# Performance work log

Measured on AMD Instinct MI355X. Metric: run time of the kernel, lower is better.

The kernel has to match this reference:

```python
import jax, jax.numpy as jnp
import numpy as np

H = 8
HID = 512
DH = HID // H
EPS = 1e-5


def _ln(x, g, b):
    mu = jnp.mean(x, axis=-1, keepdims=True)
    var = jnp.mean(jnp.square(x - mu), axis=-1, keepdims=True)
    return (x - mu) * jax.lax.rsqrt(var + EPS) * g + b


def setup_inputs() -> dict:
    key = jax.random.key(0)
    ks = jax.random.split(key, 40)
    L, M, P, D = 4096, 1024, 4096, 512

    def xav(k, shp):
        lim = np.sqrt(6.0 / (shp[0] + shp[1]))
        return jax.random.uniform(k, shp, jnp.float32, -lim, lim)

    inp = {
        'lncRNA_embedding': jax.random.normal(ks[0], (L, D), jnp.float32),
        'miRNA_embedding': jax.random.normal(ks[1], (M, D), jnp.float32),
        'protein_embedding': jax.random.normal(ks[2], (P, D), jnp.float32),
        'lncRNA_miRNA_matrix': jax.random.randint(ks[3], (L, M), 0, 2, jnp.int32),
        'protein_miRNA_matrix': jax.random.randint(ks[4], (P, M), 0, 2, jnp.int32),
    }
    names = ['Wl', 'Wm', 'Wp', 'Wql', 'Wkl', 'Wvl', 'Wqp', 'Wkp', 'Wvp']
    for i, n in enumerate(names):
        inp[n] = xav(ks[5 + i], (HID, HID))
        inp['b' + n[1:]] = jnp.zeros((HID,), jnp.float32)
    inp['Wml'] = xav(ks[20], (2 * HID, D // 2))
    inp['bml'] = jnp.zeros((D // 2,), jnp.float32)
    inp['Wmp'] = xav(ks[21], (2 * HID, D // 2))
    inp['bmp'] = jnp.zeros((D // 2,), jnp.float32)
    inp['g1'] = jnp.ones((D // 2,), jnp.float32)
    inp['be1'] = jnp.zeros((D // 2,), jnp.float32)
    inp['g2'] = jnp.ones((D // 2,), jnp.float32)
    inp['be2'] = jnp.zeros((D // 2,), jnp.float32)
    # first three linears take dim-D input (D == HID here)
    return inp


def reference(lncRNA_embedding, miRNA_embedding, protein_embedding,
              lncRNA_miRNA_matrix, protein_miRNA_matrix,
              Wl, bl, Wm, bm, Wp, bp,
              Wql, bql, Wkl, bkl, Wvl, bvl,
              Wqp, bqp, Wkp, bkp, Wvp, bvp,
              Wml, bml, Wmp, bmp, g1, be1, g2, be2):
    L = lncRNA_embedding.shape[0]
    M = miRNA_embedding.shape[0]
    P = protein_embedding.shape[0]

    lt = lncRNA_embedding @ Wl + bl          # [L, HID]
    mt = miRNA_embedding @ Wm + bm           # [M, HID]
    pt = protein_embedding @ Wp + bp         # [P, HID]

    def heads(x, W, b, n):
        return (x @ W + b).reshape(n, H, DH)

    Ql = heads(lt, Wql, bql, L)              # [L, H, DH]
    Kl = heads(mt, Wkl, bkl, M)
    Vl = heads(mt, Wvl, bvl, M)
    Qp = heads(pt, Wqp, bqp, P)
    Kp = heads(mt, Wkp, bkp, M)
    Vp = heads(mt, Wvp, bvp, M)

    scale = 1.0 / np.sqrt(DH)
    sl = jnp.einsum('lhd,mhd->hlm', Ql, Kl) * scale      # [H, L, M]
    sl = jnp.where(lncRNA_miRNA_matrix[None] == 0, -1e9, sl)
    awl = jax.nn.softmax(sl, axis=-1)

    sp = jnp.einsum('phd,mhd->hpm', Qp, Kp) * scale      # [H, P, M]
    sp = jnp.where(protein_miRNA_matrix[None] == 0, -1e9, sp)
    awp = jax.nn.softmax(sp, axis=-1)

    ctx_l = jax.nn.relu(jnp.einsum('hlm,mhd->lhd', awl, Vl).reshape(L, HID))
    ctx_p = jax.nn.relu(jnp.einsum('hpm,mhd->phd', awp, Vp).reshape(P, HID))

    mutual = jnp.einsum('hlm,hpm->lp', awl, awp) / H     # [L, P]

    fin_l = ctx_l + mutual @ ctx_p
    fin_p = ctx_p + mutual.T @ ctx_l

    out_l = _ln(jnp.concatenate([lt, fin_l], axis=-1) @ Wml + bml, g1, be1)
    out_p = _ln(jnp.concatenate([fin_p, pt], axis=-1) @ Wmp + bmp, g2, be2)
    return out_l, out_p
```

## Files before the change

kernel.cpp:

```cpp
#include <hip/hip_runtime.h>
#include <hip/hip_bf16.h>

using bf16 = __hip_bfloat16;
typedef __attribute__((ext_vector_type(8))) short short8;
typedef __attribute__((ext_vector_type(4))) float floatx4;
typedef __attribute__((ext_vector_type(8))) unsigned short ushort8;
typedef __attribute__((ext_vector_type(4))) int i32x4;
typedef __attribute__((ext_vector_type(8))) int i32x8;

__device__ __forceinline__ float b2f(unsigned short u) {
    union { unsigned int i; float f; } x; x.i = ((unsigned int)u) << 16; return x.f;
}

__device__ __forceinline__ void async16(const void* g, void* l) {
    __builtin_amdgcn_global_load_lds((const __attribute__((address_space(1))) void*)g,
                                     (__attribute__((address_space(3))) void*)l,
                                     16, 0, 0);
}

__device__ __forceinline__ unsigned char f2e4m3(float f) {
    unsigned s = (__float_as_uint(f) >> 24) & 0x80u;
    f = fminf(fabsf(f), 448.f);
    if (f < 0.015625f) {
        int d = (int)rintf(f * 512.f);
        return (unsigned char)(s | (unsigned)d);
    }
    int E = (int)((__float_as_uint(f) >> 23) & 255u) - 127;
    float ulp_inv = __uint_as_float((unsigned)(127 + 3 - E) << 23);
    int m = (int)rintf(f * ulp_inv);
    int n = (m == 16) ? ((E + 8) << 3) : (((E + 7) << 3) + (m - 8));
    if (n > 0x7E) n = 0x7E;
    return (unsigned char)(s | (unsigned)n);
}

__device__ __forceinline__ unsigned int pk4_e4m3(float a, float b, float c, float d) {
#if __has_builtin(__builtin_amdgcn_cvt_pk_fp8_f32)
    int p = __builtin_amdgcn_cvt_pk_fp8_f32(a, b, 0, false);
    p = __builtin_amdgcn_cvt_pk_fp8_f32(c, d, p, true);
    return (unsigned int)p;
#else
    return (unsigned)f2e4m3(a) | ((unsigned)f2e4m3(b) << 8) |
           ((unsigned)f2e4m3(c) << 16) | ((unsigned)f2e4m3(d) << 24);
#endif
}

__device__ __forceinline__ bool sniff_wave(const unsigned short* p) {
    const int lane = threadIdx.x & 63;
    int wild = 0;
#pragma unroll
    for (int j = 0; j < 4; ++j) {
        float a = fabsf(b2f(p[lane * 4 + j]));
        wild += !(a <= 1e4f);
    }
#pragma unroll
    for (int o = 1; o < 64; o <<= 1) wild += __shfl_xor(wild, o);
    return wild > 16;
}

struct Cvt { const void* src; bf16* dst; int n; };
struct PrepArgs {
    Cvt cv[18];
    const void* tsrc[11];
    bf16* tdst[11];
    const int* msrc[2];
    unsigned char* mdst[2];
    const unsigned short* sn;
};

__global__ __launch_bounds__(256) void prep(PrepArgs a) {
    const int y = blockIdx.y;
    __shared__ bf16 tile[32][33];

    if (y >= 29) {
        const int* src = a.msrc[y - 29];
        unsigned char* dst = a.mdst[y - 29];
        const int n = 4096 * 1024;
        const int stride = gridDim.x * 256 * 16;
        for (int i = (blockIdx.x * 256 + threadIdx.x) * 16; i < n; i += stride) {
            union { unsigned char b[16]; i32x4 v; } u;
#pragma unroll
            for (int j = 0; j < 4; ++j) {
                i32x4 m = *(const i32x4*)(src + i + j * 4);
#pragma unroll
                for (int k = 0; k < 4; ++k) u.b[j * 4 + k] = m[k] ? 1 : 0;
            }
            *(i32x4*)(dst + i) = u.v;
        }
        return;
    }

    const bool f32 = sniff_wave(a.sn);
    if (y < 18) {
        const Cvt c = a.cv[y];
        const int stride = gridDim.x * 256 * 8;
        for (int i = (blockIdx.x * 256 + threadIdx.x) * 8; i < c.n; i += stride) {
            if (f32) {
                const float* s = (const float*)c.src + i;
#pragma unroll
                for (int j = 0; j < 8; ++j) c.dst[i + j] = __float2bfloat16(s[j]);
            } else {
                *(ushort8*)((unsigned short*)c.dst + i) =
                    *(const ushort8*)((const unsigned short*)c.src + i);
            }
        }
        return;
    }

    const int tx = threadIdx.x & 31;
    const int ty = threadIdx.x >> 5;
    if (y < 27) {
        const void* in = a.tsrc[y - 18];
        bf16* out = a.tdst[y - 18];
        const int bc = (blockIdx.x & 15) * 32;
        const int br = (blockIdx.x >> 4) * 32;
#pragma unroll
        for (int i = 0; i < 32; i += 8) {
            const size_t idx = (size_t)(br + ty + i) * 512 + bc + tx;
            tile[ty + i][tx] = f32 ? __float2bfloat16(((const float*)in)[idx])
                                   : ((const bf16*)in)[idx];
        }
        __syncthreads();
#pragma unroll
        for (int i = 0; i < 32; i += 8)
            out[(size_t)(bc + ty + i) * 512 + br + tx] = tile[tx][ty + i];
    } else {
        const void* in = a.tsrc[y - 27 + 9];
        bf16* out = a.tdst[y - 27 + 9];
        const int bc = (blockIdx.x & 7) * 32;
        const int br = (blockIdx.x >> 3) * 32;
#pragma unroll
        for (int i = 0; i < 32; i += 8) {
            const size_t idx = (size_t)(br + ty + i) * 256 + bc + tx;
            tile[ty + i][tx] = f32 ? __float2bfloat16(((const float*)in)[idx])
                                   : ((const bf16*)in)[idx];
        }
        __syncthreads();
#pragma unroll
        for (int i = 0; i < 32; i += 8)
            out[(size_t)(bc + ty + i) * 1024 + br + tx] = tile[tx][ty + i];
    }
}

struct SegTab { const bf16* W[3]; const bf16* bias[3]; bf16* C[3]; int ldc[3]; int rs[3]; };

__global__ __launch_bounds__(256) void gemm_bt_seg(
    const bf16* __restrict__ A, SegTab T, int K)
{
    constexpr int TM = 2, TN = 2;
    __align__(16) __shared__ bf16 As[64 * 64];
    __align__(16) __shared__ bf16 Bs[64 * 64];

    const int lane = threadIdx.x & 63;
    const int wv   = threadIdx.x >> 6;
    const int gm   = blockIdx.y * 64;
    const int seg  = (gm >= 5120) ? 2 : ((gm >= 4096) ? 1 : 0);
    const bf16* B  = T.W[seg];
    const bf16* bias = T.bias[seg];
    bf16* C        = T.C[seg];
    const int ldc  = T.ldc[seg];
    const int m_base = gm - T.rs[seg];
    const int n_base = blockIdx.x * 64;
    const int wm0 = (wv >> 1) * 32;
    const int wn0 = (wv & 1) * 32;

    floatx4 zero = {0.f, 0.f, 0.f, 0.f};
    floatx4 acc[TM][TN];
#pragma unroll
    for (int mt = 0; mt < TM; ++mt)
#pragma unroll
        for (int nt = 0; nt < TN; ++nt) acc[mt][nt] = zero;

    const int sr  = lane >> 3;
    const int sce = ((lane & 7) ^ sr) * 8;
    const int fr  = lane & 15;
    const int q   = lane >> 4;
    const int sw  = fr & 7;

    for (int k0 = 0; k0 < K; k0 += 64) {
#pragma unroll
        for (int cc = 0; cc < 2; ++cc) {
            const int r0t = (wv + cc * 4) * 8;
            async16(A + (size_t)(gm + r0t + sr) * 512 + k0 + sce, &As[r0t * 64]);
            async16(B + (size_t)(n_base + r0t + sr) * 512 + k0 + sce, &Bs[r0t * 64]);
        }
        __syncthreads();
#pragma unroll
        for (int s = 0; s < 2; ++s) {
            const int off = ((s * 4 + q) ^ sw) * 8;
            short8 af[TM], bfr[TN];
#pragma unroll
            for (int mt = 0; mt < TM; ++mt)
                af[mt] = *(const short8*)&As[(wm0 + mt * 16 + fr) * 64 + off];
#pragma unroll
            for (int nt = 0; nt < TN; ++nt)
                bfr[nt] = *(const short8*)&Bs[(wn0 + nt * 16 + fr) * 64 + off];
#pragma unroll
            for (int mt = 0; mt < TM; ++mt)
#pragma unroll
                for (int nt = 0; nt < TN; ++nt)
                    acc[mt][nt] = __builtin_amdgcn_mfma_f32_16x16x32_bf16(
                        af[mt], bfr[nt], acc[mt][nt], 0, 0, 0);
        }
        __syncthreads();
    }

    const int er = lane >> 4;
    const int ec = lane & 15;
#pragma unroll
    for (int nt = 0; nt < TN; ++nt) {
        const int col = n_base + wn0 + nt * 16 + ec;
        const float bv = __bfloat162float(bias[col]);
#pragma unroll
        for (int mt = 0; mt < TM; ++mt)
#pragma unroll
            for (int r = 0; r < 4; ++r) {
                const int row = m_base + wm0 + mt * 16 + er * 4 + r;
                C[(size_t)row * ldc + col] = __float2bfloat16(acc[mt][nt][r] + bv);
            }
    }
}

struct BtArgs { const bf16* A; const bf16* B; void* C; const bf16* bias;
                int lda, ldb, ldc; };
struct BtSet { BtArgs s[3]; };

template <bool F32OUT, bool REMAP2>
__global__ __launch_bounds__(256) void gemm_btx(BtSet P, int K, float scale)
{
    constexpr int TM = 2, TN = 2;
    __align__(16) __shared__ bf16 As[64 * 64];
    __align__(16) __shared__ bf16 Bs[64 * 64];

    const BtArgs g = P.s[blockIdx.z];
    int bx = blockIdx.x, by = blockIdx.y;
    if (REMAP2 && blockIdx.z == 2) {
        const int flat = by * gridDim.x + bx;
        bx = flat & 31; by = flat >> 5;
    }
    const int lane = threadIdx.x & 63;
    const int wv   = threadIdx.x >> 6;
    const int m_base = by * 64;
    const int n_base = bx * 64;
    const int wm0 = (wv >> 1) * 32;
    const int wn0 = (wv & 1) * 32;

    floatx4 zero = {0.f, 0.f, 0.f, 0.f};
    floatx4 acc[TM][TN];
#pragma unroll
    for (int mt = 0; mt < TM; ++mt)
#pragma unroll
        for (int nt = 0; nt < TN; ++nt) acc[mt][nt] = zero;

    const int sr  = lane >> 3;
    const int sce = ((lane & 7) ^ sr) * 8;
    const int fr  = lane & 15;
    const int q   = lane >> 4;
    const int sw  = fr & 7;

    for (int k0 = 0; k0 < K; k0 += 64) {
#pragma unroll
        for (int cc = 0; cc < 2; ++cc) {
            const int r0t = (wv + cc * 4) * 8;
            async16(g.A + (size_t)(m_base + r0t + sr) * g.lda + k0 + sce, &As[r0t * 64]);
            async16(g.B + (size_t)(n_base + r0t + sr) * g.ldb + k0 + sce, &Bs[r0t * 64]);
        }
        __syncthreads();
#pragma unroll
        for (int s = 0; s < 2; ++s) {
            const int off = ((s * 4 + q) ^ sw) * 8;
            short8 af[TM], bfr[TN];
#pragma unroll
            for (int mt = 0; mt < TM; ++mt)
                af[mt] = *(const short8*)&As[(wm0 + mt * 16 + fr) * 64 + off];
#pragma unroll
            for (int nt = 0; nt < TN; ++nt)
                bfr[nt] = *(const short8*)&Bs[(wn0 + nt * 16 + fr) * 64 + off];
#pragma unroll
            for (int mt = 0; mt < TM; ++mt)
#pragma unroll
                for (int nt = 0; nt < TN; ++nt)
                    acc[mt][nt] = __builtin_amdgcn_mfma_f32_16x16x32_bf16(
                        af[mt], bfr[nt], acc[mt][nt], 0, 0, 0);
        }
        __syncthreads();
    }

    const int er = lane >> 4;
    const int ec = lane & 15;
#pragma unroll
    for (int nt = 0; nt < TN; ++nt) {
        const int col = n_base + wn0 + nt * 16 + ec;
        const float bv = __bfloat162float(g.bias[col]);
#pragma unroll
        for (int mt = 0; mt < TM; ++mt)
#pragma unroll
            for (int r = 0; r < 4; ++r) {
                const int row = m_base + wm0 + mt * 16 + er * 4 + r;
                const float v = acc[mt][nt][r] * scale + bv;
                if constexpr (F32OUT)
                    ((float*)g.C)[(size_t)row * g.ldc + col] = v;
                else
                    ((bf16*)g.C)[(size_t)row * g.ldc + col] = __float2bfloat16(v);
            }
    }
}

struct ScArgs { const bf16* Q; const bf16* K; const unsigned char* mask;
                unsigned char* aw; unsigned char* awt; };
struct ScSet { ScArgs s[2]; const bf16* vsrc[2]; unsigned char* vdst[2]; };

__global__ __launch_bounds__(256) void scores_v8(ScSet P, int ldk, float scale)
{
    __shared__ float wred[16][4];
    __shared__ float wsum[16][4];
    __shared__ float tile[32][33];

    const int flat = blockIdx.x;
    if (flat >= 4096) {
        const int f2   = flat - 4096;
        const int side = f2 >> 9;
        const int rem  = f2 & 511;
        const bf16* in = P.vsrc[side];
        unsigned char* out = P.vdst[side];
        const int bc = (rem & 15) * 32;
        const int br = (rem >> 4) * 32;
        const int tx = threadIdx.x & 31;
        const int ty = threadIdx.x >> 5;
#pragma unroll
        for (int i = 0; i < 32; i += 8)
            tile[ty + i][tx] =
                __bfloat162float(in[(size_t)(br + ty + i) * 2048 + bc + tx]) * 4.0f;
        __syncthreads();
        const unsigned int vp = pk4_e4m3(tile[tx][ty], tile[tx][ty + 8],
                                         tile[tx][ty + 16], tile[tx][ty + 24]);
#pragma unroll
        for (int i = 0; i < 4; ++i)
            out[(size_t)(bc + ty + i * 8) * 1024 + br + tx] =
                (unsigned char)(vp >> (8 * i));
        return;
    }

    const int side = flat >> 11;
    const int idx  = flat & 2047;
    const int h    = idx & 7;
    const int r0   = (idx >> 3) * 16;

    const ScArgs g = P.s[side];
    const int t    = threadIdx.x;
    const int lane = t & 63;
    const int w    = t >> 6;
    const int fr   = lane & 15;
    const int fq   = lane >> 4;
    const int cbase = w * 256;

    const short* Qs = (const short*)g.Q + (size_t)(r0 + fr) * 512 + h * 64 + fq * 8;
    short8 a0 = *(const short8*)(Qs);
    short8 a1 = *(const short8*)(Qs + 32);

    floatx4 accs[16];
    const short* Kb = (const short*)g.K + h * 64 + fq * 8;
#pragma unroll
    for (int c = 0; c < 16; ++c) {
        const int krow = cbase + c * 16 + fr;
        short8 b0 = *(const short8*)(Kb + (size_t)krow * ldk);
        short8 b1 = *(const short8*)(Kb + (size_t)krow * ldk + 32);
        floatx4 acc = {0.f, 0.f, 0.f, 0.f};
        acc = __builtin_amdgcn_mfma_f32_16x16x32_bf16(a0, b0, acc, 0, 0, 0);
        acc = __builtin_amdgcn_mfma_f32_16x16x32_bf16(a1, b1, acc, 0, 0, 0);
        accs[c] = acc;
    }

    float mxr[4] = {-3e38f, -3e38f, -3e38f, -3e38f};
#pragma unroll
    for (int c = 0; c < 16; ++c) {
        const int col = cbase + c * 16 + fr;
#pragma unroll
        for (int r = 0; r < 4; ++r) {
            const int row = r0 + fq * 4 + r;
            float v = (g.mask[(size_t)row * 1024 + col] == 0) ? -1e9f
                                                              : accs[c][r] * scale;
            accs[c][r] = v;
            mxr[r] = fmaxf(mxr[r], v);
        }
    }
#pragma unroll
    for (int o = 1; o < 16; o <<= 1)
#pragma unroll
        for (int r = 0; r < 4; ++r) mxr[r] = fmaxf(mxr[r], __shfl_xor(mxr[r], o));
    if (fr == 0)
#pragma unroll
        for (int r = 0; r < 4; ++r) wred[fq * 4 + r][w] = mxr[r];
    __syncthreads();

    float mx[4], sm[4] = {0.f, 0.f, 0.f, 0.f};
#pragma unroll
    for (int r = 0; r < 4; ++r) {
        const int row = fq * 4 + r;
        mx[r] = fmaxf(fmaxf(wred[row][0], wred[row][1]),
                      fmaxf(wred[row][2], wred[row][3]));
    }
#pragma unroll
    for (int c = 0; c < 16; ++c)
#pragma unroll
        for (int r = 0; r < 4; ++r) {
            float e = __expf(accs[c][r] - mx[r]);
            accs[c][r] = e;
            sm[r] += e;
        }
#pragma unroll
    for (int o = 1; o < 16; o <<= 1)
#pragma unroll
        for (int r = 0; r < 4; ++r) sm[r] += __shfl_xor(sm[r], o);
    if (fr == 0)
#pragma unroll
        for (int r = 0; r < 4; ++r) wsum[fq * 4 + r][w] = sm[r];
    __syncthreads();

    float inv[4];
#pragma unroll
    for (int r = 0; r < 4; ++r) {
        const int row = fq * 4 + r;
        inv[r] = 32.0f / (wsum[row][0] + wsum[row][1] + wsum[row][2] + wsum[row][3]);
    }
    unsigned char* awtb = g.awt + (size_t)(r0 >> 4) * 131072 + fq * 4;
#pragma unroll
    for (int c = 0; c < 16; ++c) {
        const int col = cbase + c * 16 + fr;
        const unsigned int pk = pk4_e4m3(accs[c][0] * inv[0], accs[c][1] * inv[1],
                                         accs[c][2] * inv[2], accs[c][3] * inv[3]);
#pragma unroll
        for (int r = 0; r < 4; ++r)
            g.aw[(size_t)(r0 + fq * 4 + r) * 8192 + h * 1024 + col] =
                (unsigned char)(pk >> (8 * r));
        *(unsigned int*)(awtb + (size_t)(h * 1024 + col) * 16) = pk;
    }
}

struct B8Args { const unsigned char* A; const unsigned char* B; bf16* C;
                unsigned char* CT; };
struct B8Pair { B8Args s[2]; };

__global__ __launch_bounds__(256) void gemm_bt8_ctx(
    B8Pair P, int lda, long long a_kshift, int ldb, int ldc, int ldct,
    int K, float scale)
{
    constexpr int TM = 2, TN = 2;
    __align__(16) __shared__ unsigned char As[2][64 * 64];
    __align__(16) __shared__ unsigned char Bs[2][64 * 64];

    const B8Args g = P.s[blockIdx.z];
    const int lane = threadIdx.x & 63;
    const int wv   = threadIdx.x >> 6;
    const int m_base = blockIdx.y * 64;
    const int n_base = blockIdx.x * 64;
    const unsigned char* A = g.A + (long long)blockIdx.x * a_kshift;

    const int wm0 = (wv >> 1) * 32;
    const int wn0 = (wv & 1) * 32;

    floatx4 zero = {0.f, 0.f, 0.f, 0.f};
    floatx4 acc[TM][TN];
#pragma unroll
    for (int mt = 0; mt < TM; ++mt)
#pragma unroll
        for (int nt = 0; nt < TN; ++nt) acc[mt][nt] = zero;

    const int ar = lane >> 2;
    const int ac = (((lane & 3) ^ (ar & 3)) * 16);
    const int fr = lane & 15;
    const int q  = lane >> 4;
    const int sw = fr & 3;

    const int NT = K >> 6;

    auto stage = [&](int tt, int b) {
        const int k0 = tt << 6;
        async16(A + (size_t)(m_base + wv * 16 + ar) * lda + k0 + ac,
                &As[b][wv * 16 * 64]);
        async16(g.B + (size_t)(n_base + wv * 16 + ar) * ldb + k0 + ac,
                &Bs[b][wv * 16 * 64]);
    };

    stage(0, 0);
    stage(1, 1);

    for (int t = 0; t < NT; ++t) {
        const int cur = t & 1;
        if (t + 1 < NT)
            asm volatile("s_waitcnt vmcnt(2)\n\ts_barrier" ::: "memory");
        else
            asm volatile("s_waitcnt vmcnt(0)\n\ts_barrier" ::: "memory");

#pragma unroll
        for (int s = 0; s < 2; ++s) {
            const int boff = (((s * 2 + (q >> 1)) ^ sw) * 16) + (q & 1) * 8;
            long af[TM], bfr[TN];
#pragma unroll
            for (int mt = 0; mt < TM; ++mt)
                af[mt] = *(const long*)&As[cur][(wm0 + mt * 16 + fr) * 64 + boff];
#pragma unroll
            for (int nt = 0; nt < TN; ++nt)
                bfr[nt] = *(const long*)&Bs[cur][(wn0 + nt * 16 + fr) * 64 + boff];
#pragma unroll
            for (int mt = 0; mt < TM; ++mt)
#pragma unroll
                for (int nt = 0; nt < TN; ++nt)
                    acc[mt][nt] = __builtin_amdgcn_mfma_f32_16x16x32_fp8_fp8(
                        af[mt], bfr[nt], acc[mt][nt], 0, 0, 0);
        }
        asm volatile("s_barrier" ::: "memory");
        if (t + 2 < NT) stage(t + 2, cur);
    }

    const int er = lane >> 4;
    const int ec = lane & 15;
#pragma unroll
    for (int nt = 0; nt < TN; ++nt) {
        const int col = n_base + wn0 + nt * 16 + ec;
#pragma unroll
        for (int mt = 0; mt < TM; ++mt) {
            const int rowb = m_base + wm0 + mt * 16 + er * 4;
            float v0 = fmaxf(acc[mt][nt][0] * scale, 0.f);
            float v1 = fmaxf(acc[mt][nt][1] * scale, 0.f);
            float v2 = fmaxf(acc[mt][nt][2] * scale, 0.f);
            float v3 = fmaxf(acc[mt][nt][3] * scale, 0.f);
            g.C[(size_t)(rowb + 0) * ldc + col] = __float2bfloat16(v0);
            g.C[(size_t)(rowb + 1) * ldc + col] = __float2bfloat16(v1);
            g.C[(size_t)(rowb + 2) * ldc + col] = __float2bfloat16(v2);
            g.C[(size_t)(rowb + 3) * ldc + col] = __float2bfloat16(v3);
            const unsigned int pk = pk4_e4m3(v0 * 16.f, v1 * 16.f, v2 * 16.f, v3 * 16.f);
            *(unsigned int*)(g.CT + (size_t)col * ldct + rowb) = pk;
        }
    }
}

struct MxArgs { const unsigned char* A; const unsigned char* B; void* C;
                const bf16* Cz; unsigned char* CT; };
struct MxPair { MxArgs s[2]; };

template <int BM, int BN, bool ADDC0, bool FP8OUT, bool TOUT, bool DBUF>
__global__ __launch_bounds__(256, 2) void gemm_bt8mx(
    MxPair P, int lda, int ldb, int ldbk, int ldc, int ldc0, int ldct,
    int K, float scale)
{
    constexpr int WM = BM / 2;
    constexpr int WN = BN / 2;
    constexpr int TM = WM / 16;
    constexpr int TN = WN / 16;
    static_assert(!DBUF || (BM / 32 + BN / 32) == 8, "DBUF assumes vmcnt(8)");

    __align__(16) __shared__ unsigned char As[(DBUF ? 2 : 1) * BM * 128];
    __align__(16) __shared__ unsigned char Bs[(DBUF ? 2 : 1) * BN * 128];

    const MxArgs g = P.s[blockIdx.z];
    const int lane = threadIdx.x & 63;
    const int wv   = threadIdx.x >> 6;
    const int m_base = blockIdx.y * BM;
    const int n_base = blockIdx.x * BN;

    const int wm0 = (wv >> 1) * WM;
    const int wn0 = (wv & 1) * WN;

    floatx4 zero = {0.f, 0.f, 0.f, 0.f};
    floatx4 acc[TM][TN];
#pragma unroll
    for (int mt = 0; mt < TM; ++mt)
#pragma unroll
        for (int nt = 0; nt < TN; ++nt) acc[mt][nt] = zero;

    const int sr = lane >> 3;
    const int sc = ((lane & 7) ^ sr) * 16;
    const int fr = lane & 15;
    const int q  = lane >> 4;
    const int sw = fr & 7;

    auto stage = [&](int k0, int b) {
        unsigned char* Ab = As + b * (BM * 128);
        unsigned char* Bb = Bs + b * (BN * 128);
#pragma unroll
        for (int cc = 0; cc < BM / 32; ++cc) {
            const int r0t = (wv + cc * 4) * 8;
            async16(g.A + (size_t)(m_base + r0t + sr) * lda + k0 + sc, Ab + r0t * 128);
        }
#pragma unroll
        for (int cc = 0; cc < BN / 32; ++cc) {
            const int r0t = (wv + cc * 4) * 8;
            async16(g.B + (size_t)(n_base + r0t + sr) * ldb +
                        (size_t)((k0 + sc) >> 4) * ldbk, Bb + r0t * 128);
        }
    };

    auto compute = [&](int b) {
        const unsigned char* Ab = As + b * (BM * 128);
        const unsigned char* Bb = Bs + b * (BN * 128);
        i32x8 bfr[TN];
#pragma unroll
        for (int nt = 0; nt < TN; ++nt) {
            const unsigned char* rp = &Bb[(wn0 + nt * 16 + fr) * 128];
            i32x4 lo = *(const i32x4*)(rp + (((q * 2 + 0) ^ sw) * 16));
            i32x4 hi = *(const i32x4*)(rp + (((q * 2 + 1) ^ sw) * 16));
            bfr[nt] = __builtin_shufflevector(lo, hi, 0, 1, 2, 3, 4, 5, 6, 7);
        }
#pragma unroll
        for (int mt = 0; mt < TM; ++mt) {
            const unsigned char* rp = &Ab[(wm0 + mt * 16 + fr) * 128];
            i32x4 lo = *(const i32x4*)(rp + (((q * 2 + 0) ^ sw) * 16));
            i32x4 hi = *(const i32x4*)(rp + (((q * 2 + 1) ^ sw) * 16));
            i32x8 af = __builtin_shufflevector(lo, hi, 0, 1, 2, 3, 4, 5, 6, 7);
#pragma unroll
            for (int nt = 0; nt < TN; ++nt)
                acc[mt][nt] = __builtin_amdgcn_mfma_scale_f32_16x16x128_f8f6f4(
                    af, bfr[nt], acc[mt][nt], 0, 0, 0, 127, 0, 127);
        }
    };

    if constexpr (DBUF) {
        const int NT = K >> 7;
        stage(0, 0);
        stage(128, 1);
        for (int t = 0; t < NT; ++t) {
            const int cur = t & 1;
            if (t + 1 < NT)
                asm volatile("s_waitcnt vmcnt(8)\n\ts_barrier" ::: "memory");
            else
                asm volatile("s_waitcnt vmcnt(0)\n\ts_barrier" ::: "memory");
            compute(cur);
            asm volatile("s_barrier" ::: "memory");
            if (t + 2 < NT) stage((t + 2) << 7, cur);
        }
    } else {
        for (int k0 = 0; k0 < K; k0 += 128) {
            stage(k0, 0);
            __syncthreads();
            compute(0);
            __syncthreads();
        }
    }

    const int er = lane >> 4;
    const int ec = lane & 15;
#pragma unroll
    for (int nt = 0; nt < TN; ++nt) {
        const int col = n_base + wn0 + nt * 16 + ec;
#pragma unroll
        for (int mt = 0; mt < TM; ++mt) {
            const int rowb = m_base + wm0 + mt * 16 + er * 4;
            float v[4];
#pragma unroll
            for (int r = 0; r < 4; ++r) {
                v[r] = acc[mt][nt][r] * scale;
                if constexpr (ADDC0)
                    v[r] += __bfloat162float(g.Cz[(size_t)(rowb + r) * ldc0 + col]);
            }
            if constexpr (FP8OUT) {
                const unsigned int pk = pk4_e4m3(v[0], v[1], v[2], v[3]);
#pragma unroll
                for (int r = 0; r < 4; ++r)
                    ((unsigned char*)g.C)[(size_t)(rowb + r) * ldc + col] =
                        (unsigned char)(pk >> (8 * r));
                if constexpr (TOUT)
                    *(unsigned int*)(g.CT + (size_t)col * ldct + rowb) = pk;
            } else {
#pragma unroll
                for (int r = 0; r < 4; ++r)
                    ((bf16*)g.C)[(size_t)(rowb + r) * ldc + col] = __float2bfloat16(v[r]);
            }
        }
    }
}

__global__ __launch_bounds__(256) void ln_all(
    const float* __restrict__ X,
    const bf16* __restrict__ g1, const bf16* __restrict__ be1,
    const bf16* __restrict__ g2, const bf16* __restrict__ be2,
    void* __restrict__ out, const unsigned short* __restrict__ sn)
{
    const bool f32 = sniff_wave(sn);
    const int lane = threadIdx.x & 63;
    const int wv   = threadIdx.x >> 6;
    const int row  = blockIdx.x * 4 + wv;
    const bf16* gg = (row >= 4096) ? g2 : g1;
    const bf16* bb = (row >= 4096) ? be2 : be1;
    const float* x = X + (size_t)row * 256;
    float v[4], s = 0.f, s2 = 0.f;
#pragma unroll
    for (int i = 0; i < 4; ++i) {
        v[i] = x[lane + 64 * i];
        s += v[i]; s2 += v[i] * v[i];
    }
#pragma unroll
    for (int o = 1; o < 64; o <<= 1) { s += __shfl_xor(s, o); s2 += __shfl_xor(s2, o); }
    const float mu  = s * (1.0f / 256.0f);
    const float var = fmaxf(s2 * (1.0f / 256.0f) - mu * mu, 0.0f);
    const float inv = rsqrtf(var + 1e-5f);
#pragma unroll
    for (int i = 0; i < 4; ++i) {
        const int c = lane + 64 * i;
        const float y = (v[i] - mu) * inv * __bfloat162float(gg[c]) + __bfloat162float(bb[c]);
        if (f32) ((float*)out)[(size_t)row * 256 + c] = y;
        else     ((bf16*)out)[(size_t)row * 256 + c] = __float2bfloat16(y);
    }
}

extern "C" void kernel_launch(void* const* d_in, const int* in_sizes, int n_in,
                              void* d_out, int out_size, void* d_ws, size_t ws_size,
                              hipStream_t stream)
{
    const int L = 4096, Mm = 1024, P = 4096;

    const int* mask_l = (const int*)d_in[3];
    const int* mask_p = (const int*)d_in[4];
    const unsigned short* sn = (const unsigned short*)d_in[0];

    char* ws = (char*)d_ws;
    size_t off = 0;
    auto alloc = [&](size_t bytes) {
        void* p = ws + off; off += (bytes + 255) & ~(size_t)255; return p;
    };

    bf16* wt_all = (bf16*)alloc((size_t)9 * 512 * 512 * 2);
    bf16* WmlT   = (bf16*)alloc(1024 * 256 * 2);
    bf16* WmpT   = (bf16*)alloc(1024 * 256 * 2);
    bf16* b_l    = (bf16*)alloc(512 * 2);
    bf16* b_m    = (bf16*)alloc(512 * 2);
    bf16* b_p    = (bf16*)alloc(512 * 2);
    bf16* b_ql   = (bf16*)alloc(512 * 2);
    bf16* b_qp   = (bf16*)alloc(512 * 2);
    bf16* bcat   = (bf16*)alloc(2048 * 2);
    bf16* bml_c  = (bf16*)alloc(256 * 2);
    bf16* bmp_c  = (bf16*)alloc(256 * 2);
    bf16* g1c    = (bf16*)alloc(256 * 2);
    bf16* be1c   = (bf16*)alloc(256 * 2);
    bf16* g2c    = (bf16*)alloc(256 * 2);
    bf16* be2c   = (bf16*)alloc(256 * 2);
    bf16* emb_all = (bf16*)alloc((size_t)(L + Mm + P) * 512 * 2);
    bf16* embl   = emb_all;
    bf16* embm   = emb_all + (size_t)L * 512;
    bf16* embp   = embm + (size_t)Mm * 512;
    bf16* cat_l  = (bf16*)alloc((size_t)L * 1024 * 2);
    bf16* cat_p  = (bf16*)alloc((size_t)P * 1024 * 2);
    bf16* mt     = (bf16*)alloc((size_t)Mm * 512 * 2);
    bf16* Ql     = (bf16*)alloc((size_t)L * 512 * 2);
    bf16* Qp     = (bf16*)alloc((size_t)P * 512 * 2);
    bf16* kvcat  = (bf16*)alloc((size_t)Mm * 2048 * 2);
    unsigned char* V8lT = (unsigned char*)alloc((size_t)512 * Mm);
    unsigned char* V8pT = (unsigned char*)alloc((size_t)512 * Mm);
    bf16* ctx_l  = (bf16*)alloc((size_t)L * 512 * 2);
    bf16* ctx_p  = (bf16*)alloc((size_t)P * 512 * 2);
    unsigned char* ctx8lT = (unsigned char*)alloc((size_t)512 * L);
    unsigned char* ctx8pT = (unsigned char*)alloc((size_t)512 * P);
    unsigned char* awlT8  = (unsigned char*)alloc((size_t)8192 * 4096);
    unsigned char* awpT8  = (unsigned char*)alloc((size_t)8192 * 4096);
    unsigned char* awl8 = (unsigned char*)alloc((size_t)L * 8192);
    unsigned char* awp8 = (unsigned char*)alloc((size_t)P * 8192);
    unsigned char* m8l  = (unsigned char*)alloc((size_t)L * 1024);
    unsigned char* m8p  = (unsigned char*)alloc((size_t)P * 1024);
    unsigned char* T1lT = (unsigned char*)emb_all;
    unsigned char* T1pT = (unsigned char*)emb_all + (size_t)512 * 8192;
    float* tmp1 = (float*)awp8;

    PrepArgs pa;
    pa.sn = sn;
    pa.cv[0]  = { d_in[0],  embl, L * 512 };
    pa.cv[1]  = { d_in[1],  embm, Mm * 512 };
    pa.cv[2]  = { d_in[2],  embp, P * 512 };
    pa.cv[3]  = { d_in[6],  b_l,  512 };
    pa.cv[4]  = { d_in[8],  b_m,  512 };
    pa.cv[5]  = { d_in[10], b_p,  512 };
    pa.cv[6]  = { d_in[12], b_ql, 512 };
    pa.cv[7]  = { d_in[18], b_qp, 512 };
    pa.cv[8]  = { d_in[14], bcat,        512 };
    pa.cv[9]  = { d_in[16], bcat + 512,  512 };
    pa.cv[10] = { d_in[20], bcat + 1024, 512 };
    pa.cv[11] = { d_in[22], bcat + 1536, 512 };
    pa.cv[12] = { d_in[24], bml_c, 256 };
    pa.cv[13] = { d_in[26], bmp_c, 256 };
    pa.cv[14] = { d_in[27], g1c,  256 };
    pa.cv[15] = { d_in[28], be1c, 256 };
    pa.cv[16] = { d_in[29], g2c,  256 };
    pa.cv[17] = { d_in[30], be2c, 256 };
    const int slot_of[9] = {0, 1, 2, 3, 5, 6, 4, 7, 8};
    for (int i = 0; i < 9; ++i) {
        pa.tsrc[i] = d_in[5 + 2 * i];
        pa.tdst[i] = wt_all + (size_t)slot_of[i] * 512 * 512;
    }
    pa.tsrc[9]  = d_in[23]; pa.tdst[9]  = WmlT;
    pa.tsrc[10] = d_in[25]; pa.tdst[10] = WmpT;
    pa.msrc[0] = mask_l; pa.mdst[0] = m8l;
    pa.msrc[1] = mask_p; pa.mdst[1] = m8p;
    prep<<<dim3(256, 31), 256, 0, stream>>>(pa);

    bf16* WlT  = wt_all;
    bf16* WmT  = wt_all + (size_t)1 * 512 * 512;
    bf16* WpT  = wt_all + (size_t)2 * 512 * 512;
    bf16* WqlT = wt_all + (size_t)3 * 512 * 512;
    bf16* WqpT = wt_all + (size_t)4 * 512 * 512;
    bf16* WkvT = wt_all + (size_t)5 * 512 * 512;

    SegTab st;
    st.W[0] = WlT;  st.bias[0] = b_l; st.C[0] = cat_l;       st.ldc[0] = 1024; st.rs[0] = 0;
    st.W[1] = WmT;  st.bias[1] = b_m; st.C[1] = mt;          st.ldc[1] = 512;  st.rs[1] = 4096;
    st.W[2] = WpT;  st.bias[2] = b_p; st.C[2] = cat_p + 512; st.ldc[2] = 1024; st.rs[2] = 5120;
    gemm_bt_seg<<<dim3(8, 144), 256, 0, stream>>>(emb_all, st, 512);

    BtSet qs;
    qs.s[0] = { cat_l,       WqlT, Ql,    b_ql, 1024, 512, 512 };
    qs.s[1] = { cat_p + 512, WqpT, Qp,    b_qp, 1024, 512, 512 };
    qs.s[2] = { mt,          WkvT, kvcat, bcat, 512,  512, 2048 };
    gemm_btx<false, true><<<dim3(8, 64, 3), 256, 0, stream>>>(qs, 512, 1.0f);

    ScSet sc;
    sc.s[0] = { Ql, kvcat,        m8l, awl8, awlT8 };
    sc.s[1] = { Qp, kvcat + 1024, m8p, awp8, awpT8 };
    sc.vsrc[0] = kvcat + 512;  sc.vdst[0] = V8lT;
    sc.vsrc[1] = kvcat + 1536; sc.vdst[1] = V8pT;
    scores_v8<<<dim3(5120), 256, 0, stream>>>(sc, 2048, 0.125f);

    B8Pair cx = { { { awl8, V8lT, ctx_l, ctx8lT },
                    { awp8, V8pT, ctx_p, ctx8pT } } };
    gemm_bt8_ctx<<<dim3(8, 64, 2), 256, 0, stream>>>(
        cx, 8192, 1024, 1024, 512, 4096, 1024, 1.0f / 128.0f);

    MxPair t1 = { { { ctx8pT, awpT8, T1lT, nullptr, nullptr },
                    { ctx8lT, awlT8, T1pT, nullptr, nullptr } } };
    gemm_bt8mx<512, 64, false, true, false, false><<<dim3(128, 1, 2), 256, 0, stream>>>(
        t1, 4096, 16, 131072, 8192, 0, 0, 4096, 1.0f / 128.0f);

    MxPair fn = { { { awl8, T1lT, cat_l + 512, ctx_l, nullptr },
                    { awp8, T1pT, cat_p,       ctx_p, nullptr } } };
    gemm_bt8mx<128, 128, true, false, false, true><<<dim3(4, 32, 2), 256, 0, stream>>>(
        fn, 8192, 8192, 16, 1024, 512, 0, 8192, 1.0f / 1024.0f);

    BtSet fp;
    fp.s[0] = { cat_l, WmlT, tmp1,                   bml_c, 1024, 1024, 256 };
    fp.s[1] = { cat_p, WmpT, tmp1 + (size_t)L * 256, bmp_c, 1024, 1024, 256 };
    fp.s[2] = fp.s[0];
    gemm_btx<true, false><<<dim3(4, 64, 2), 256, 0, stream>>>(fp, 1024, 1.0f);

    ln_all<<<dim3(2048), 256, 0, stream>>>(tmp1, g1c, be1c, g2c, be2c, d_out, sn);
}
```

Baseline: 453.2 us.

## Transpose mask to column-major and coalesce attention-weight stores via LDS byte permute

The prep kernel now writes the int-to-byte mask transposed ([M][L]) through an LDS tile, so the scores kernel can load four row-mask bytes for a column with one 32-bit load instead of four scattered byte loads. The scores kernel also stages packed fp8 attention weights in a per-wave LDS buffer and uses byte permutes to emit 32-bit row-contiguous stores to aw instead of single-byte scattered writes. This adds 16 KB of LDS per block, which may lower occupancy, and turns the mask conversion into a tiled transpose with extra barriers.

```diff
diff --git a/kernel.cpp b/kernel.cpp
--- a/kernel.cpp
+++ b/kernel.cpp
@@ -44,6 +44,20 @@
 #endif
 }
 
+__device__ __forceinline__ unsigned int perm4(unsigned v0, unsigned v1,
+                                              unsigned v2, unsigned v3, int rr) {
+#if __has_builtin(__builtin_amdgcn_perm)
+    const unsigned sel = (unsigned)rr | ((unsigned)(rr + 4) << 8);
+    const unsigned t01 = __builtin_amdgcn_perm(v1, v0, sel);
+    const unsigned t23 = __builtin_amdgcn_perm(v3, v2, sel);
+    return __builtin_amdgcn_perm(t23, t01, 0x05040100u);
+#else
+    const int s = 8 * rr;
+    return ((v0 >> s) & 255u) | (((v1 >> s) & 255u) << 8) |
+           (((v2 >> s) & 255u) << 16) | (((v3 >> s) & 255u) << 24);
+#endif
+}
+
 __device__ __forceinline__ bool sniff_wave(const unsigned short* p) {
     const int lane = threadIdx.x & 63;
     int wild = 0;
@@ -70,21 +84,25 @@
 __global__ __launch_bounds__(256) void prep(PrepArgs a) {
     const int y = blockIdx.y;
     __shared__ bf16 tile[32][33];
+    __shared__ unsigned char mt8[32][36];
 
     if (y >= 29) {
         const int* src = a.msrc[y - 29];
         unsigned char* dst = a.mdst[y - 29];
-        const int n = 4096 * 1024;
-        const int stride = gridDim.x * 256 * 16;
-        for (int i = (blockIdx.x * 256 + threadIdx.x) * 16; i < n; i += stride) {
-            union { unsigned char b[16]; i32x4 v; } u;
-#pragma unroll
-            for (int j = 0; j < 4; ++j) {
-                i32x4 m = *(const i32x4*)(src + i + j * 4);
-#pragma unroll
-                for (int k = 0; k < 4; ++k) u.b[j * 4 + k] = m[k] ? 1 : 0;
-            }
-            *(i32x4*)(dst + i) = u.v;
+        const int tx = threadIdx.x & 31;
+        const int ty = threadIdx.x >> 5;
+        for (int tt = 0; tt < 16; ++tt) {
+            const int tid = blockIdx.x * 16 + tt;
+            const int r0 = (tid >> 5) * 32;
+            const int c0 = (tid & 31) * 32;
+#pragma unroll
+            for (int i = 0; i < 32; i += 8)
+                mt8[ty + i][tx] = src[(size_t)(r0 + ty + i) * 1024 + c0 + tx] ? 1 : 0;
+            __syncthreads();
+#pragma unroll
+            for (int i = 0; i < 32; i += 8)
+                dst[(size_t)(c0 + ty + i) * 4096 + r0 + tx] = mt8[tx][ty + i];
+            __syncthreads();
         }
         return;
     }
@@ -314,6 +332,7 @@
     __shared__ float wred[16][4];
     __shared__ float wsum[16][4];
     __shared__ float tile[32][33];
+    __shared__ unsigned int tbuf[4096];
 
     const int flat = blockIdx.x;
     if (flat >= 4096) {
@@ -374,11 +393,11 @@
 #pragma unroll
     for (int c = 0; c < 16; ++c) {
         const int col = cbase + c * 16 + fr;
+        const unsigned int mu =
+            *(const unsigned int*)(g.mask + (size_t)col * 4096 + r0 + fq * 4);
 #pragma unroll
         for (int r = 0; r < 4; ++r) {
-            const int row = r0 + fq * 4 + r;
-            float v = (g.mask[(size_t)row * 1024 + col] == 0) ? -1e9f
-                                                              : accs[c][r] * scale;
+            float v = (((mu >> (8 * r)) & 255u) == 0) ? -1e9f : accs[c][r] * scale;
             accs[c][r] = v;
             mxr[r] = fmaxf(mxr[r], v);
         }
@@ -423,16 +442,25 @@
         inv[r] = 32.0f / (wsum[row][0] + wsum[row][1] + wsum[row][2] + wsum[row][3]);
     }
     unsigned char* awtb = g.awt + (size_t)(r0 >> 4) * 131072 + fq * 4;
+    unsigned int* tb = &tbuf[w * 1024];
 #pragma unroll
     for (int c = 0; c < 16; ++c) {
         const int col = cbase + c * 16 + fr;
         const unsigned int pk = pk4_e4m3(accs[c][0] * inv[0], accs[c][1] * inv[1],
                                          accs[c][2] * inv[2], accs[c][3] * inv[3]);
-#pragma unroll
-        for (int r = 0; r < 4; ++r)
-            g.aw[(size_t)(r0 + fq * 4 + r) * 8192 + h * 1024 + col] =
-                (unsigned char)(pk >> (8 * r));
+        tb[fq * 256 + c * 16 + fr] = pk;
         *(unsigned int*)(awtb + (size_t)(h * 1024 + col) * 16) = pk;
+    }
+    unsigned char* awb = g.aw + (size_t)(r0 + fq * 4) * 8192 + h * 1024 + cbase;
+#pragma unroll
+    for (int tt = 0; tt < 4; ++tt) {
+        const int j = tt * 16 + fr;
+        const i32x4 v = *(const i32x4*)&tb[fq * 256 + 4 * j];
+#pragma unroll
+        for (int rr = 0; rr < 4; ++rr)
+            *(unsigned int*)(awb + (size_t)rr * 8192 + 4 * j) =
+                perm4((unsigned)v[0], (unsigned)v[1], (unsigned)v[2],
+                      (unsigned)v[3], rr);
     }
 }
 
@@ -753,8 +781,8 @@
     unsigned char* awpT8  = (unsigned char*)alloc((size_t)8192 * 4096);
     unsigned char* awl8 = (unsigned char*)alloc((size_t)L * 8192);
     unsigned char* awp8 = (unsigned char*)alloc((size_t)P * 8192);
-    unsigned char* m8l  = (unsigned char*)alloc((size_t)L * 1024);
-    unsigned char* m8p  = (unsigned char*)alloc((size_t)P * 1024);
+    unsigned char* m8l  = (unsigned char*)alloc((size_t)1024 * 4096);
+    unsigned char* m8p  = (unsigned char*)alloc((size_t)1024 * 4096);
     unsigned char* T1lT = (unsigned char*)emb_all;
     unsigned char* T1pT = (unsigned char*)emb_all + (size_t)512 * 8192;
     float* tmp1 = (float*)awp8;
```

New measurement: 471.7 us. +4.1%, slower.
